# Kernel optimization log

Hardware: AMD Instinct MI355X
Metric: run time of the kernel (lower is better)

## Reference

```python
import jax, jax.numpy as jnp
import numpy as np

N_HEADS = 16
D_MODEL = 2048
D_HEAD = D_MODEL // N_HEADS
B, T = 4, 2048


def setup_inputs() -> dict:
    key = jax.random.key(0)
    k1, k2, k3 = jax.random.split(key, 3)
    x = jax.random.normal(k1, (B, T, D_MODEL), dtype=jnp.float32)
    # stored as [in, out] so y = x @ W + b (equivalent to torch Linear with W_torch = W.T)
    W_qkv = jax.random.normal(k2, (D_MODEL, 3 * D_MODEL), dtype=jnp.float32) * (D_MODEL ** -0.5)
    b_qkv = jnp.zeros((3 * D_MODEL,), dtype=jnp.float32)
    W_out = jax.random.normal(k3, (D_MODEL, D_MODEL), dtype=jnp.float32) * (D_MODEL ** -0.5)
    b_out = jnp.zeros((D_MODEL,), dtype=jnp.float32)
    return {"x": x, "W_qkv": W_qkv, "b_qkv": b_qkv, "W_out": W_out, "b_out": b_out}


def reference(x, W_qkv, b_qkv, W_out, b_out):
    b, t, c = x.shape
    qkv = x @ W_qkv + b_qkv                       # [B,T,3C]
    q, k, v = jnp.split(qkv, 3, axis=-1)
    # [B,T,C] -> [B,H,T,Dh]
    def heads(u):
        return u.reshape(b, t, N_HEADS, D_HEAD).transpose(0, 2, 1, 3)
    q, k, v = heads(q), heads(k), heads(v)
    scale = 1.0 / D_HEAD                          # muP scale: 1/d_head (not 1/sqrt)
    att = jnp.einsum('bhqd,bhkd->bhqk', q, k) * scale
    causal = jnp.tril(jnp.ones((t, t), dtype=bool))
    att = jnp.where(causal, att, -jnp.inf)
    att = jax.nn.softmax(att, axis=-1)
    y = jnp.einsum('bhqk,bhkd->bhqd', att, v)     # [B,H,T,Dh]
    y = y.transpose(0, 2, 1, 3).reshape(b, t, c)
    return y @ W_out + b_out
```

## Files before the change

kernel.cpp:

```cpp
#include <hip/hip_runtime.h>
#include <hip/hip_bf16.h>
#include <cstdint>


using f32x4  = __attribute__((ext_vector_type(4))) float;
using u32x4  = __attribute__((ext_vector_type(4))) unsigned int;
using u16x8  = __attribute__((ext_vector_type(8))) unsigned short;
using u16x4  = __attribute__((ext_vector_type(4))) unsigned short;
using bf16x8 = __attribute__((ext_vector_type(8))) __bf16;

__device__ __forceinline__ unsigned short f2bf(float f) {
  unsigned int u = __builtin_bit_cast(unsigned int, f);
  u += 0x7fffu + ((u >> 16) & 1u);
  return (unsigned short)(u >> 16);
}

__device__ __forceinline__ void async_copy16(const unsigned short* g, unsigned short* l) {
  __builtin_amdgcn_global_load_lds(
      (const __attribute__((address_space(1))) unsigned int*)g,
      (__attribute__((address_space(3))) unsigned int*)l,
      16, 0, 0);
}

__global__ __launch_bounds__(256) void cast_x_kernel(const float* __restrict__ x,
                                                     unsigned short* __restrict__ xb) {
  const size_t i = (size_t)blockIdx.x * 256 + threadIdx.x;
  const float* p = x + i * 8;
  f32x4 a = *(const f32x4*)p;
  f32x4 b = *(const f32x4*)(p + 4);
  u16x8 o;
#pragma unroll
  for (int e = 0; e < 4; ++e) { o[e] = f2bf(a[e]); o[e + 4] = f2bf(b[e]); }
  *(u32x4*)(xb + i * 8) = __builtin_bit_cast(u32x4, o);
}

__global__ __launch_bounds__(256) void transpose_cast_w(const float* __restrict__ W,
                                                        unsigned short* __restrict__ WT,
                                                        int K, int N) {
  __shared__ unsigned short tbuf[64 * 68];
  const int tid = threadIdx.x;
  const int k0 = blockIdx.x * 64, n0 = blockIdx.y * 64;
#pragma unroll
  for (int it = 0; it < 4; ++it) {
    int c = it * 256 + tid;
    int kl = c >> 4, n4 = (c & 15) * 4;
    f32x4 v = *(const f32x4*)(W + (size_t)(k0 + kl) * N + n0 + n4);
#pragma unroll
    for (int e = 0; e < 4; ++e) tbuf[(n4 + e) * 68 + kl] = f2bf(v[e]);
  }
  __syncthreads();
#pragma unroll
  for (int it = 0; it < 2; ++it) {
    int c = it * 256 + tid;
    int nl = c >> 3, k8 = (c & 7) * 8;
    u16x4 lo = *(const u16x4*)&tbuf[nl * 68 + k8];
    u16x4 hi = *(const u16x4*)&tbuf[nl * 68 + k8 + 4];
    u16x8 o;
#pragma unroll
    for (int e = 0; e < 4; ++e) { o[e] = lo[e]; o[e + 4] = hi[e]; }
    *(u32x4*)(WT + (size_t)(n0 + nl) * K + k0 + k8) = __builtin_bit_cast(u32x4, o);
  }
}

__global__ __launch_bounds__(256) void transpose_v_kernel(const unsigned short* __restrict__ qkv,
                                                          unsigned short* __restrict__ vT) {
  __shared__ unsigned short tbuf[64 * 68];
  const int tid = threadIdx.x;
  const int t0 = blockIdx.x * 64;
  const int d0 = blockIdx.y * 64;
  const int bh = blockIdx.z;
  const int b = bh >> 4, h = bh & 15;
#pragma unroll
  for (int it = 0; it < 2; ++it) {
    int c = it * 256 + tid;
    int tl = c >> 3, d8 = (c & 7) * 8;
    u32x4 v = *(const u32x4*)(qkv + (size_t)(b * 2048 + t0 + tl) * 6144 + 4096 + h * 128 + d0 + d8);
    u16x8 u = __builtin_bit_cast(u16x8, v);
#pragma unroll
    for (int e = 0; e < 8; ++e) tbuf[(d8 + e) * 68 + tl] = u[e];
  }
  __syncthreads();
#pragma unroll
  for (int it = 0; it < 2; ++it) {
    int c = it * 256 + tid;
    int dl = c >> 3, t8 = (c & 7) * 8;
    u16x4 lo = *(const u16x4*)&tbuf[dl * 68 + t8];
    u16x4 hi = *(const u16x4*)&tbuf[dl * 68 + t8 + 4];
    u16x8 o;
#pragma unroll
    for (int e = 0; e < 4; ++e) { o[e] = lo[e]; o[e + 4] = hi[e]; }
    *(u32x4*)(vT + ((size_t)bh * 128 + d0 + dl) * 2048 + t0 + t8) = __builtin_bit_cast(u32x4, o);
  }
}


__device__ __forceinline__ void stage_region(const unsigned short* gsrc, int K,
                                             unsigned short* region, int tid) {
#pragma unroll
  for (int l = 0; l < 2; ++l) {
    const int s = l * 512 + tid;
    const int row = s >> 3, c = s & 7;
    const int g = c ^ (row & 7);
    async_copy16(gsrc + (size_t)row * K + g * 8, region + s * 8);
  }
}

__device__ __forceinline__ bf16x8 lds_frag(const unsigned short* region, int row, int ch) {
  return __builtin_bit_cast(bf16x8,
      *(const u32x4*)(region + row * 64 + ((ch ^ (row & 7)) * 8)));
}

template <bool OUT_BF16>
__global__ __launch_bounds__(512, 1) void gemm_bt(const unsigned short* __restrict__ A,
                                                  const unsigned short* __restrict__ BT,
                                                  const float* __restrict__ bias,
                                                  void* __restrict__ Cout,
                                                  int M, int N, int K) {
  __shared__ unsigned short As[32768];
  __shared__ unsigned short Bs[32768];

  const int tid  = threadIdx.x;
  const int lane = tid & 63;
  const int wave = tid >> 6;
  const int r16  = lane & 15;
  const int quad = lane >> 4;
  const int wm   = (wave >> 2) * 128;
  const int wn   = (wave & 3) * 64;
  const int rhA  = wave >> 2;
  const int rhB  = (wave >> 1) & 1;
  const int brow = wn & 64;

  const int orig = blockIdx.y * gridDim.x + blockIdx.x;
  const int xcd  = orig & 7;
  const int kb   = orig >> 3;
  const int MC   = gridDim.x >> 3;
  const int m0   = (xcd * MC + (kb % MC)) * 256;
  const int n0   = (kb / MC) * 256;

  const unsigned short* Ag = A + (size_t)m0 * K;
  const unsigned short* Bg = BT + (size_t)n0 * K;
  const int NT = K >> 6;

  f32x4 acc[8][4] = {};

#pragma unroll
  for (int tt = 0; tt < 2; ++tt) {
    const size_t kk0 = (size_t)tt * 64;
    unsigned short* Ad = As + tt * 16384;
    unsigned short* Bd = Bs + tt * 16384;
    stage_region(Bg + kk0, K, Bd, tid);
    stage_region(Bg + (size_t)128 * K + kk0, K, Bd + 8192, tid);
    stage_region(Ag + kk0, K, Ad, tid);
    stage_region(Ag + (size_t)128 * K + kk0, K, Ad + 8192, tid);
  }
  asm volatile("s_waitcnt vmcnt(8)" ::: "memory");
  __builtin_amdgcn_s_barrier();

  for (int t = 0; t < NT; ++t) {
    const int buf = t & 1;
    const unsigned short* Ar = As + buf * 16384 + rhA * 8192;
    const unsigned short* Br = Bs + buf * 16384 + rhB * 8192;
    unsigned short* Asg = As + buf * 16384;
    unsigned short* Bsg = Bs + buf * 16384;
    const bool pre = (t + 2 < NT);
    const size_t kpre = (size_t)(t + 2) << 6;

    bf16x8 a0[4][2], a1[4][2], b0[2][2], b1[2][2];

#pragma unroll
    for (int mi = 0; mi < 4; ++mi)
#pragma unroll
      for (int kk = 0; kk < 2; ++kk)
        a0[mi][kk] = lds_frag(Ar, mi * 16 + r16, kk * 4 + quad);
#pragma unroll
    for (int nj = 0; nj < 2; ++nj)
#pragma unroll
      for (int kk = 0; kk < 2; ++kk)
        b0[nj][kk] = lds_frag(Br, brow + nj * 16 + r16, kk * 4 + quad);
    __builtin_amdgcn_s_barrier();
    asm volatile("s_waitcnt lgkmcnt(0)" ::: "memory");
    __builtin_amdgcn_sched_barrier(0);
    __builtin_amdgcn_s_setprio(1);
#pragma unroll
    for (int mi = 0; mi < 4; ++mi)
#pragma unroll
      for (int nj = 0; nj < 2; ++nj)
#pragma unroll
        for (int kk = 0; kk < 2; ++kk)
          acc[mi][nj] = __builtin_amdgcn_mfma_f32_16x16x32_bf16(a0[mi][kk], b0[nj][kk], acc[mi][nj], 0, 0, 0);
    __builtin_amdgcn_s_setprio(0);
    __builtin_amdgcn_s_barrier();

#pragma unroll
    for (int nj = 0; nj < 2; ++nj)
#pragma unroll
      for (int kk = 0; kk < 2; ++kk)
        b1[nj][kk] = lds_frag(Br, brow + 32 + nj * 16 + r16, kk * 4 + quad);
    __builtin_amdgcn_s_barrier();
    asm volatile("s_waitcnt lgkmcnt(0)" ::: "memory");
    __builtin_amdgcn_sched_barrier(0);
    __builtin_amdgcn_s_setprio(1);
#pragma unroll
    for (int mi = 0; mi < 4; ++mi)
#pragma unroll
      for (int nj = 0; nj < 2; ++nj)
#pragma unroll
        for (int kk = 0; kk < 2; ++kk)
          acc[mi][nj + 2] = __builtin_amdgcn_mfma_f32_16x16x32_bf16(a0[mi][kk], b1[nj][kk], acc[mi][nj + 2], 0, 0, 0);
    __builtin_amdgcn_s_setprio(0);
    __builtin_amdgcn_s_barrier();

#pragma unroll
    for (int mi = 0; mi < 4; ++mi)
#pragma unroll
      for (int kk = 0; kk < 2; ++kk)
        a1[mi][kk] = lds_frag(Ar, 64 + mi * 16 + r16, kk * 4 + quad);
    if (pre) {
      stage_region(Bg + kpre, K, Bsg, tid);
      stage_region(Bg + (size_t)128 * K + kpre, K, Bsg + 8192, tid);
    }
    __builtin_amdgcn_s_barrier();
    asm volatile("s_waitcnt lgkmcnt(0)" ::: "memory");
    __builtin_amdgcn_sched_barrier(0);
    __builtin_amdgcn_s_setprio(1);
#pragma unroll
    for (int mi = 0; mi < 4; ++mi)
#pragma unroll
      for (int nj = 0; nj < 2; ++nj)
#pragma unroll
        for (int kk = 0; kk < 2; ++kk)
          acc[mi + 4][nj + 2] = __builtin_amdgcn_mfma_f32_16x16x32_bf16(a1[mi][kk], b1[nj][kk], acc[mi + 4][nj + 2], 0, 0, 0);
    __builtin_amdgcn_s_setprio(0);
    __builtin_amdgcn_s_barrier();

    if (pre) {
      stage_region(Ag + kpre, K, Asg, tid);
      stage_region(Ag + (size_t)128 * K + kpre, K, Asg + 8192, tid);
    }
    __builtin_amdgcn_s_barrier();
    __builtin_amdgcn_sched_barrier(0);
    __builtin_amdgcn_s_setprio(1);
#pragma unroll
    for (int mi = 0; mi < 4; ++mi)
#pragma unroll
      for (int nj = 0; nj < 2; ++nj)
#pragma unroll
        for (int kk = 0; kk < 2; ++kk)
          acc[mi + 4][nj] = __builtin_amdgcn_mfma_f32_16x16x32_bf16(a1[mi][kk], b0[nj][kk], acc[mi + 4][nj], 0, 0, 0);
    __builtin_amdgcn_s_setprio(0);
    if (pre) { asm volatile("s_waitcnt vmcnt(8)" ::: "memory"); }
    else     { asm volatile("s_waitcnt vmcnt(0)" ::: "memory"); }
    __builtin_amdgcn_s_barrier();
  }

#pragma unroll
  for (int nj = 0; nj < 4; ++nj) {
    const int n = n0 + wn + nj * 16 + r16;
    const float bv = bias[n];
#pragma unroll
    for (int mi = 0; mi < 8; ++mi) {
      const int mr = m0 + wm + mi * 16 + quad * 4;
#pragma unroll
      for (int r = 0; r < 4; ++r) {
        float v = acc[mi][nj][r] + bv;
        if constexpr (OUT_BF16)
          ((unsigned short*)Cout)[(size_t)(mr + r) * N + n] = f2bf(v);
        else
          ((float*)Cout)[(size_t)(mr + r) * N + n] = v;
      }
    }
  }
}

__global__ __launch_bounds__(256, 2) void attn_kernel(const unsigned short* __restrict__ qkv,
                                                      const unsigned short* __restrict__ vT,
                                                      unsigned short* __restrict__ y) {
  __shared__ unsigned short Ks[64 * 128];
  __shared__ unsigned short Vs[128 * 64];
  __shared__ unsigned short Ps[4][32 * 72];

  const int tid  = threadIdx.x;
  const int lane = tid & 63;
  const int wave = tid >> 6;
  const int r16  = lane & 15;
  const int quad = lane >> 4;
  const int qt   = 15 - blockIdx.y;
  const int q0   = qt * 128;
  const int bh   = blockIdx.x;
  const int b    = bh >> 4, h = bh & 15;
  const int wq0  = q0 + wave * 32;
  unsigned short* pl = Ps[wave];

  bf16x8 aq[2][4];
#pragma unroll
  for (int mi = 0; mi < 2; ++mi) {
    const unsigned short* qp = qkv + (size_t)(b * 2048 + wq0 + mi * 16 + r16) * 6144 + h * 128;
#pragma unroll
    for (int kc = 0; kc < 4; ++kc)
      aq[mi][kc] = __builtin_bit_cast(bf16x8, *(const u32x4*)(qp + kc * 32 + quad * 8));
  }

  f32x4 o[2][8] = {};
  float rs_l[2][4] = {};

  const unsigned short* kbase = qkv + (size_t)b * 2048 * 6144 + 2048 + h * 128;
  const unsigned short* vbase = vT + (size_t)bh * 128 * 2048;
  const int ntiles = 2 * qt + 2;

  const int kg = (tid & 15) ^ (tid >> 4);
  const int vg = (tid & 7) ^ ((tid >> 3) & 7);
  const int krow0 = tid >> 4;
  const int vrow0 = tid >> 3;

  u32x4 kreg[4], vreg[4];

#define ATTN_LOADREGS(KV0)                                                              \
  {                                                                                     \
    _Pragma("unroll")                                                                   \
    for (int it = 0; it < 4; ++it)                                                      \
      kreg[it] = *(const u32x4*)(kbase + (size_t)((KV0) + it * 16 + krow0) * 6144 + kg * 8); \
    _Pragma("unroll")                                                                   \
    for (int it = 0; it < 4; ++it)                                                      \
      vreg[it] = *(const u32x4*)(vbase + (size_t)(it * 32 + vrow0) * 2048 + (KV0) + vg * 8); \
  }

  ATTN_LOADREGS(0);

  for (int t = 0; t < ntiles; ++t) {
    const int kv0 = t * 64;
    asm volatile("s_waitcnt vmcnt(0)" ::: "memory");
    __builtin_amdgcn_s_barrier();
    __builtin_amdgcn_sched_barrier(0);
#pragma unroll
    for (int it = 0; it < 4; ++it)
      *(u32x4*)(Ks + (it * 256 + tid) * 8) = kreg[it];
#pragma unroll
    for (int it = 0; it < 4; ++it)
      *(u32x4*)(Vs + (it * 256 + tid) * 8) = vreg[it];
    asm volatile("s_waitcnt lgkmcnt(0)" ::: "memory");
    if (t + 1 < ntiles) ATTN_LOADREGS(kv0 + 64);
    __builtin_amdgcn_s_barrier();
    __builtin_amdgcn_sched_barrier(0);

    f32x4 s[2][4] = {};
#pragma unroll
    for (int kc = 0; kc < 4; ++kc) {
#pragma unroll
      for (int nt = 0; nt < 4; ++nt) {
        const int krow = nt * 16 + r16;
        const int chunk = kc * 4 + quad;
        bf16x8 bk = __builtin_bit_cast(bf16x8,
            *(const u32x4*)(Ks + (krow * 16 + (chunk ^ (krow & 15))) * 8));
#pragma unroll
        for (int mi = 0; mi < 2; ++mi)
          s[mi][nt] = __builtin_amdgcn_mfma_f32_16x16x32_bf16(aq[mi][kc], bk, s[mi][nt], 0, 0, 0);
      }
    }

    const bool need_mask = (kv0 + 64 > wq0);
#pragma unroll
    for (int mi = 0; mi < 2; ++mi) {
#pragma unroll
      for (int r = 0; r < 4; ++r) {
        const int qg = wq0 + mi * 16 + quad * 4 + r;
        float acc = 0.0f;
#pragma unroll
        for (int nt = 0; nt < 4; ++nt) {
          float e = exp2f(s[mi][nt][r] * 0.0112718764f);
          if (need_mask && (kv0 + nt * 16 + r16 > qg)) e = 0.0f;
          acc += e;
          pl[(mi * 16 + quad * 4 + r) * 72 + nt * 16 + r16] = f2bf(e);
        }
        rs_l[mi][r] += acc;
      }
    }

#pragma unroll
    for (int kc = 0; kc < 2; ++kc) {
      bf16x8 ap[2];
#pragma unroll
      for (int mi = 0; mi < 2; ++mi)
        ap[mi] = __builtin_bit_cast(bf16x8,
            *(const u32x4*)(pl + (mi * 16 + r16) * 72 + kc * 32 + quad * 8));
#pragma unroll
      for (int d = 0; d < 8; ++d) {
        const int drow = d * 16 + r16;
        const int chunk = kc * 4 + quad;
        bf16x8 bv = __builtin_bit_cast(bf16x8,
            *(const u32x4*)(Vs + (drow * 8 + (chunk ^ (drow & 7))) * 8));
#pragma unroll
        for (int mi = 0; mi < 2; ++mi)
          o[mi][d] = __builtin_amdgcn_mfma_f32_16x16x32_bf16(ap[mi], bv, o[mi][d], 0, 0, 0);
      }
    }
  }

#pragma unroll
  for (int mi = 0; mi < 2; ++mi) {
#pragma unroll
    for (int r = 0; r < 4; ++r) {
      float rs = rs_l[mi][r];
#pragma unroll
      for (int off = 8; off >= 1; off >>= 1) rs += __shfl_xor(rs, off);
      const float inv = 1.0f / rs;
      const int qg = wq0 + mi * 16 + quad * 4 + r;
      unsigned short* yp = y + (size_t)(b * 2048 + qg) * 2048 + h * 128;
#pragma unroll
      for (int d = 0; d < 8; ++d)
        yp[d * 16 + r16] = f2bf(o[mi][d][r] * inv);
    }
  }
#undef ATTN_LOADREGS
}

extern "C" void kernel_launch(void* const* d_in, const int* in_sizes, int n_in,
                              void* d_out, int out_size, void* d_ws, size_t ws_size,
                              hipStream_t stream) {
  const float* x     = (const float*)d_in[0];
  const float* W_qkv = (const float*)d_in[1];
  const float* b_qkv = (const float*)d_in[2];
  const float* W_out = (const float*)d_in[3];
  const float* b_out = (const float*)d_in[4];

  unsigned short* ws  = (unsigned short*)d_ws;
  unsigned short* qkv = ws;
  unsigned short* vT  = ws + 50331648;
  unsigned short* xb  = ws + 67108864;
  unsigned short* wqT = ws + 83886080;
  unsigned short* woT = ws + 96468992;
  unsigned short* y   = xb;

  cast_x_kernel<<<8192, 256, 0, stream>>>(x, xb);
  transpose_cast_w<<<dim3(32, 96), 256, 0, stream>>>(W_qkv, wqT, 2048, 6144);
  transpose_cast_w<<<dim3(32, 32), 256, 0, stream>>>(W_out, woT, 2048, 2048);
  gemm_bt<true><<<dim3(32, 24), 512, 0, stream>>>(xb, wqT, b_qkv, qkv, 8192, 6144, 2048);
  transpose_v_kernel<<<dim3(32, 2, 64), 256, 0, stream>>>(qkv, vT);
  attn_kernel<<<dim3(64, 16), 256, 0, stream>>>(qkv, vT, y);
  gemm_bt<false><<<dim3(32, 8), 512, 0, stream>>>(y, woT, b_out, d_out, 8192, 2048, 2048);
}
```

Baseline: 574.4 us.

## Software-pipeline LDS fragment loads across GEMM k-iterations

Restructures the GEMM main loop so the LDS fragment reads for each MFMA phase are issued before the previous phase's MFMAs. Next-iteration a0/b0 fragments are prefetched from the other buffer during the current iteration, and the explicit lgkmcnt waits are dropped. The global-load wait moves earlier (vmcnt(4) after the B prefetch) so the next buffer is ready before its fragments are read. This aims to hide LDS latency behind MFMA work, at the cost of more registers (a0n/b0n) and subtler buffer-hazard ordering.

Measured after the change: 1.222 ms. 2.13x slower.

```diff
diff --git a/kernel.cpp b/kernel.cpp
--- a/kernel.cpp
+++ b/kernel.cpp
@@ -156,30 +156,43 @@
   asm volatile("s_waitcnt vmcnt(8)" ::: "memory");
   __builtin_amdgcn_s_barrier();
 
+  bf16x8 a0[4][2], b0[2][2];
+  {
+    const unsigned short* Ar0 = As + rhA * 8192;
+    const unsigned short* Br0 = Bs + rhB * 8192;
+#pragma unroll
+    for (int mi = 0; mi < 4; ++mi)
+#pragma unroll
+      for (int kk = 0; kk < 2; ++kk)
+        a0[mi][kk] = lds_frag(Ar0, mi * 16 + r16, kk * 4 + quad);
+#pragma unroll
+    for (int nj = 0; nj < 2; ++nj)
+#pragma unroll
+      for (int kk = 0; kk < 2; ++kk)
+        b0[nj][kk] = lds_frag(Br0, brow + nj * 16 + r16, kk * 4 + quad);
+  }
+
   for (int t = 0; t < NT; ++t) {
     const int buf = t & 1;
-    const unsigned short* Ar = As + buf * 16384 + rhA * 8192;
-    const unsigned short* Br = Bs + buf * 16384 + rhB * 8192;
+    const unsigned short* Ar  = As + buf * 16384 + rhA * 8192;
+    const unsigned short* Br  = Bs + buf * 16384 + rhB * 8192;
+    const unsigned short* Arn = As + (buf ^ 1) * 16384 + rhA * 8192;
+    const unsigned short* Brn = Bs + (buf ^ 1) * 16384 + rhB * 8192;
     unsigned short* Asg = As + buf * 16384;
     unsigned short* Bsg = Bs + buf * 16384;
     const bool pre = (t + 2 < NT);
+    const bool nx  = (t + 1 < NT);
     const size_t kpre = (size_t)(t + 2) << 6;
 
-    bf16x8 a0[4][2], a1[4][2], b0[2][2], b1[2][2];
-
-#pragma unroll
-    for (int mi = 0; mi < 4; ++mi)
+    bf16x8 a1[4][2], b1[2][2], a0n[4][2], b0n[2][2];
+
+    __builtin_amdgcn_s_barrier();
+    __builtin_amdgcn_sched_barrier(0);
+#pragma unroll
+    for (int nj = 0; nj < 2; ++nj)
 #pragma unroll
       for (int kk = 0; kk < 2; ++kk)
-        a0[mi][kk] = lds_frag(Ar, mi * 16 + r16, kk * 4 + quad);
-#pragma unroll
-    for (int nj = 0; nj < 2; ++nj)
-#pragma unroll
-      for (int kk = 0; kk < 2; ++kk)
-        b0[nj][kk] = lds_frag(Br, brow + nj * 16 + r16, kk * 4 + quad);
-    __builtin_amdgcn_s_barrier();
-    asm volatile("s_waitcnt lgkmcnt(0)" ::: "memory");
-    __builtin_amdgcn_sched_barrier(0);
+        b1[nj][kk] = lds_frag(Br, brow + 32 + nj * 16 + r16, kk * 4 + quad);
     __builtin_amdgcn_s_setprio(1);
 #pragma unroll
     for (int mi = 0; mi < 4; ++mi)
@@ -189,16 +202,15 @@
         for (int kk = 0; kk < 2; ++kk)
           acc[mi][nj] = __builtin_amdgcn_mfma_f32_16x16x32_bf16(a0[mi][kk], b0[nj][kk], acc[mi][nj], 0, 0, 0);
     __builtin_amdgcn_s_setprio(0);
-    __builtin_amdgcn_s_barrier();
-
-#pragma unroll
-    for (int nj = 0; nj < 2; ++nj)
+    __builtin_amdgcn_sched_barrier(0);
+
+    __builtin_amdgcn_s_barrier();
+    __builtin_amdgcn_sched_barrier(0);
+#pragma unroll
+    for (int mi = 0; mi < 4; ++mi)
 #pragma unroll
       for (int kk = 0; kk < 2; ++kk)
-        b1[nj][kk] = lds_frag(Br, brow + 32 + nj * 16 + r16, kk * 4 + quad);
-    __builtin_amdgcn_s_barrier();
-    asm volatile("s_waitcnt lgkmcnt(0)" ::: "memory");
-    __builtin_amdgcn_sched_barrier(0);
+        a1[mi][kk] = lds_frag(Ar, 64 + mi * 16 + r16, kk * 4 + quad);
     __builtin_amdgcn_s_setprio(1);
 #pragma unroll
     for (int mi = 0; mi < 4; ++mi)
@@ -208,20 +220,26 @@
         for (int kk = 0; kk < 2; ++kk)
           acc[mi][nj + 2] = __builtin_amdgcn_mfma_f32_16x16x32_bf16(a0[mi][kk], b1[nj][kk], acc[mi][nj + 2], 0, 0, 0);
     __builtin_amdgcn_s_setprio(0);
-    __builtin_amdgcn_s_barrier();
-
-#pragma unroll
-    for (int mi = 0; mi < 4; ++mi)
-#pragma unroll
-      for (int kk = 0; kk < 2; ++kk)
-        a1[mi][kk] = lds_frag(Ar, 64 + mi * 16 + r16, kk * 4 + quad);
+    __builtin_amdgcn_sched_barrier(0);
+
+    __builtin_amdgcn_s_barrier();
+    __builtin_amdgcn_sched_barrier(0);
     if (pre) {
       stage_region(Bg + kpre, K, Bsg, tid);
       stage_region(Bg + (size_t)128 * K + kpre, K, Bsg + 8192, tid);
-    }
-    __builtin_amdgcn_s_barrier();
-    asm volatile("s_waitcnt lgkmcnt(0)" ::: "memory");
-    __builtin_amdgcn_sched_barrier(0);
+      asm volatile("s_waitcnt vmcnt(4)" ::: "memory");
+    } else {
+      asm volatile("s_waitcnt vmcnt(0)" ::: "memory");
+    }
+    __builtin_amdgcn_s_barrier();
+    __builtin_amdgcn_sched_barrier(0);
+    if (nx) {
+#pragma unroll
+      for (int nj = 0; nj < 2; ++nj)
+#pragma unroll
+        for (int kk = 0; kk < 2; ++kk)
+          b0n[nj][kk] = lds_frag(Brn, brow + nj * 16 + r16, kk * 4 + quad);
+    }
     __builtin_amdgcn_s_setprio(1);
 #pragma unroll
     for (int mi = 0; mi < 4; ++mi)
@@ -231,14 +249,21 @@
         for (int kk = 0; kk < 2; ++kk)
           acc[mi + 4][nj + 2] = __builtin_amdgcn_mfma_f32_16x16x32_bf16(a1[mi][kk], b1[nj][kk], acc[mi + 4][nj + 2], 0, 0, 0);
     __builtin_amdgcn_s_setprio(0);
-    __builtin_amdgcn_s_barrier();
-
+    __builtin_amdgcn_sched_barrier(0);
+
+    __builtin_amdgcn_s_barrier();
+    __builtin_amdgcn_sched_barrier(0);
     if (pre) {
       stage_region(Ag + kpre, K, Asg, tid);
       stage_region(Ag + (size_t)128 * K + kpre, K, Asg + 8192, tid);
     }
-    __builtin_amdgcn_s_barrier();
-    __builtin_amdgcn_sched_barrier(0);
+    if (nx) {
+#pragma unroll
+      for (int mi = 0; mi < 4; ++mi)
+#pragma unroll
+        for (int kk = 0; kk < 2; ++kk)
+          a0n[mi][kk] = lds_frag(Arn, mi * 16 + r16, kk * 4 + quad);
+    }
     __builtin_amdgcn_s_setprio(1);
 #pragma unroll
     for (int mi = 0; mi < 4; ++mi)
@@ -248,9 +273,20 @@
         for (int kk = 0; kk < 2; ++kk)
           acc[mi + 4][nj] = __builtin_amdgcn_mfma_f32_16x16x32_bf16(a1[mi][kk], b0[nj][kk], acc[mi + 4][nj], 0, 0, 0);
     __builtin_amdgcn_s_setprio(0);
-    if (pre) { asm volatile("s_waitcnt vmcnt(8)" ::: "memory"); }
-    else     { asm volatile("s_waitcnt vmcnt(0)" ::: "memory"); }
-    __builtin_amdgcn_s_barrier();
+    __builtin_amdgcn_sched_barrier(0);
+
+    if (nx) {
+#pragma unroll
+      for (int mi = 0; mi < 4; ++mi)
+#pragma unroll
+        for (int kk = 0; kk < 2; ++kk)
+          a0[mi][kk] = a0n[mi][kk];
+#pragma unroll
+      for (int nj = 0; nj < 2; ++nj)
+#pragma unroll
+        for (int kk = 0; kk < 2; ++kk)
+          b0[nj][kk] = b0n[nj][kk];
+    }
   }
 
 #pragma unroll
```

## Halve GEMM K-tile to 32 and prefetch next-tile fragments across iterations

Applied to the files above, without the earlier changes.

Cuts the GEMM's K step from 64 to 32, which halves LDS buffer size, and changes the swizzle to suit 32-wide rows. The main loop is restructured so the a0/b0 fragments for the next tile are loaded from the other buffer while the current MFMAs run, which removes several barriers and lgkmcnt waits per step. The intent is better overlap of LDS reads and global loads with MFMA work. In exchange the loop runs twice as many iterations with less MFMA work per barrier, and it relies on implicit wait insertion for the LDS reads.

New measurement: 679.7 us. 1.18x slower.

```diff
diff --git a/kernel.cpp b/kernel.cpp
--- a/kernel.cpp
+++ b/kernel.cpp
@@ -94,20 +94,16 @@
 }
 
 
-__device__ __forceinline__ void stage_region(const unsigned short* gsrc, int K,
-                                             unsigned short* region, int tid) {
-#pragma unroll
-  for (int l = 0; l < 2; ++l) {
-    const int s = l * 512 + tid;
-    const int row = s >> 3, c = s & 7;
-    const int g = c ^ (row & 7);
-    async_copy16(gsrc + (size_t)row * K + g * 8, region + s * 8);
-  }
-}
-
-__device__ __forceinline__ bf16x8 lds_frag(const unsigned short* region, int row, int ch) {
-  return __builtin_bit_cast(bf16x8,
-      *(const u32x4*)(region + row * 64 + ((ch ^ (row & 7)) * 8)));
+__device__ __forceinline__ void stage_region32(const unsigned short* gsrc, int K,
+                                               unsigned short* region, int tid) {
+  const int row = tid >> 2, c = tid & 3;
+  const int g = c ^ ((row >> 1) & 3);
+  async_copy16(gsrc + (size_t)row * K + g * 8, region + tid * 8);
+}
+
+__device__ __forceinline__ bf16x8 lds_frag32(const unsigned short* region, int row, int q) {
+  const int ch = q ^ ((row >> 1) & 3);
+  return __builtin_bit_cast(bf16x8, *(const u32x4*)(region + row * 32 + ch * 8));
 }
 
 template <bool OUT_BF16>
@@ -116,8 +112,8 @@
                                                   const float* __restrict__ bias,
                                                   void* __restrict__ Cout,
                                                   int M, int N, int K) {
-  __shared__ unsigned short As[32768];
-  __shared__ unsigned short Bs[32768];
+  __shared__ unsigned short As[16384];
+  __shared__ unsigned short Bs[16384];
 
   const int tid  = threadIdx.x;
   const int lane = tid & 63;
@@ -139,118 +135,114 @@
 
   const unsigned short* Ag = A + (size_t)m0 * K;
   const unsigned short* Bg = BT + (size_t)n0 * K;
-  const int NT = K >> 6;
+  const int NT = K >> 5;
 
   f32x4 acc[8][4] = {};
 
 #pragma unroll
   for (int tt = 0; tt < 2; ++tt) {
-    const size_t kk0 = (size_t)tt * 64;
-    unsigned short* Ad = As + tt * 16384;
-    unsigned short* Bd = Bs + tt * 16384;
-    stage_region(Bg + kk0, K, Bd, tid);
-    stage_region(Bg + (size_t)128 * K + kk0, K, Bd + 8192, tid);
-    stage_region(Ag + kk0, K, Ad, tid);
-    stage_region(Ag + (size_t)128 * K + kk0, K, Ad + 8192, tid);
-  }
-  asm volatile("s_waitcnt vmcnt(8)" ::: "memory");
+    const size_t kk0 = (size_t)tt * 32;
+    unsigned short* Ad = As + tt * 8192;
+    unsigned short* Bd = Bs + tt * 8192;
+    stage_region32(Bg + kk0, K, Bd, tid);
+    stage_region32(Bg + (size_t)128 * K + kk0, K, Bd + 4096, tid);
+    stage_region32(Ag + kk0, K, Ad, tid);
+    stage_region32(Ag + (size_t)128 * K + kk0, K, Ad + 4096, tid);
+  }
+  asm volatile("s_waitcnt vmcnt(4)" ::: "memory");
   __builtin_amdgcn_s_barrier();
+  __builtin_amdgcn_sched_barrier(0);
+
+  bf16x8 a0[4], b0[2];
+#pragma unroll
+  for (int mi = 0; mi < 4; ++mi) a0[mi] = lds_frag32(As + rhA * 4096, mi * 16 + r16, quad);
+#pragma unroll
+  for (int nj = 0; nj < 2; ++nj) b0[nj] = lds_frag32(Bs + rhB * 4096, brow + nj * 16 + r16, quad);
 
   for (int t = 0; t < NT; ++t) {
     const int buf = t & 1;
-    const unsigned short* Ar = As + buf * 16384 + rhA * 8192;
-    const unsigned short* Br = Bs + buf * 16384 + rhB * 8192;
-    unsigned short* Asg = As + buf * 16384;
-    unsigned short* Bsg = Bs + buf * 16384;
+    const unsigned short* Ar  = As + buf * 8192 + rhA * 4096;
+    const unsigned short* Br  = Bs + buf * 8192 + rhB * 4096;
+    const unsigned short* Arn = As + (buf ^ 1) * 8192 + rhA * 4096;
+    const unsigned short* Brn = Bs + (buf ^ 1) * 8192 + rhB * 4096;
+    unsigned short* Asg = As + buf * 8192;
+    unsigned short* Bsg = Bs + buf * 8192;
     const bool pre = (t + 2 < NT);
-    const size_t kpre = (size_t)(t + 2) << 6;
-
-    bf16x8 a0[4][2], a1[4][2], b0[2][2], b1[2][2];
-
+    const bool nx  = (t + 1 < NT);
+    const size_t kpre = (size_t)(t + 2) << 5;
+
+    bf16x8 a1[4], b1[2], a0n[4], b0n[2];
+
+#pragma unroll
+    for (int nj = 0; nj < 2; ++nj) b1[nj] = lds_frag32(Br, brow + 32 + nj * 16 + r16, quad);
+    __builtin_amdgcn_s_setprio(1);
 #pragma unroll
     for (int mi = 0; mi < 4; ++mi)
 #pragma unroll
-      for (int kk = 0; kk < 2; ++kk)
-        a0[mi][kk] = lds_frag(Ar, mi * 16 + r16, kk * 4 + quad);
-#pragma unroll
-    for (int nj = 0; nj < 2; ++nj)
-#pragma unroll
-      for (int kk = 0; kk < 2; ++kk)
-        b0[nj][kk] = lds_frag(Br, brow + nj * 16 + r16, kk * 4 + quad);
+      for (int nj = 0; nj < 2; ++nj)
+        acc[mi][nj] = __builtin_amdgcn_mfma_f32_16x16x32_bf16(a0[mi], b0[nj], acc[mi][nj], 0, 0, 0);
+    __builtin_amdgcn_s_setprio(0);
+
+#pragma unroll
+    for (int mi = 0; mi < 4; ++mi) a1[mi] = lds_frag32(Ar, 64 + mi * 16 + r16, quad);
+    __builtin_amdgcn_s_setprio(1);
+#pragma unroll
+    for (int mi = 0; mi < 4; ++mi)
+#pragma unroll
+      for (int nj = 0; nj < 2; ++nj)
+        acc[mi][nj + 2] = __builtin_amdgcn_mfma_f32_16x16x32_bf16(a0[mi], b1[nj], acc[mi][nj + 2], 0, 0, 0);
+    __builtin_amdgcn_s_setprio(0);
+    __builtin_amdgcn_sched_barrier(0);
+
     __builtin_amdgcn_s_barrier();
-    asm volatile("s_waitcnt lgkmcnt(0)" ::: "memory");
-    __builtin_amdgcn_sched_barrier(0);
+    __builtin_amdgcn_sched_barrier(0);
+    if (pre) {
+      stage_region32(Bg + kpre, K, Bsg, tid);
+      stage_region32(Bg + (size_t)128 * K + kpre, K, Bsg + 4096, tid);
+      asm volatile("s_waitcnt vmcnt(2)" ::: "memory");
+    } else {
+      asm volatile("s_waitcnt vmcnt(0)" ::: "memory");
+    }
+    __builtin_amdgcn_s_barrier();
+    __builtin_amdgcn_sched_barrier(0);
+    if (nx) {
+#pragma unroll
+      for (int nj = 0; nj < 2; ++nj) b0n[nj] = lds_frag32(Brn, brow + nj * 16 + r16, quad);
+    }
     __builtin_amdgcn_s_setprio(1);
 #pragma unroll
     for (int mi = 0; mi < 4; ++mi)
 #pragma unroll
       for (int nj = 0; nj < 2; ++nj)
-#pragma unroll
-        for (int kk = 0; kk < 2; ++kk)
-          acc[mi][nj] = __builtin_amdgcn_mfma_f32_16x16x32_bf16(a0[mi][kk], b0[nj][kk], acc[mi][nj], 0, 0, 0);
+        acc[mi + 4][nj + 2] = __builtin_amdgcn_mfma_f32_16x16x32_bf16(a1[mi], b1[nj], acc[mi + 4][nj + 2], 0, 0, 0);
     __builtin_amdgcn_s_setprio(0);
+    __builtin_amdgcn_sched_barrier(0);
+
     __builtin_amdgcn_s_barrier();
-
-#pragma unroll
-    for (int nj = 0; nj < 2; ++nj)
-#pragma unroll
-      for (int kk = 0; kk < 2; ++kk)
-        b1[nj][kk] = lds_frag(Br, brow + 32 + nj * 16 + r16, kk * 4 + quad);
-    __builtin_amdgcn_s_barrier();
-    asm volatile("s_waitcnt lgkmcnt(0)" ::: "memory");
-    __builtin_amdgcn_sched_barrier(0);
+    __builtin_amdgcn_sched_barrier(0);
+    if (pre) {
+      stage_region32(Ag + kpre, K, Asg, tid);
+      stage_region32(Ag + (size_t)128 * K + kpre, K, Asg + 4096, tid);
+    }
+    if (nx) {
+#pragma unroll
+      for (int mi = 0; mi < 4; ++mi) a0n[mi] = lds_frag32(Arn, mi * 16 + r16, quad);
+    }
     __builtin_amdgcn_s_setprio(1);
 #pragma unroll
     for (int mi = 0; mi < 4; ++mi)
 #pragma unroll
       for (int nj = 0; nj < 2; ++nj)
-#pragma unroll
-        for (int kk = 0; kk < 2; ++kk)
-          acc[mi][nj + 2] = __builtin_amdgcn_mfma_f32_16x16x32_bf16(a0[mi][kk], b1[nj][kk], acc[mi][nj + 2], 0, 0, 0);
+        acc[mi + 4][nj] = __builtin_amdgcn_mfma_f32_16x16x32_bf16(a1[mi], b0[nj], acc[mi + 4][nj], 0, 0, 0);
     __builtin_amdgcn_s_setprio(0);
-    __builtin_amdgcn_s_barrier();
-
-#pragma unroll
-    for (int mi = 0; mi < 4; ++mi)
-#pragma unroll
-      for (int kk = 0; kk < 2; ++kk)
-        a1[mi][kk] = lds_frag(Ar, 64 + mi * 16 + r16, kk * 4 + quad);
-    if (pre) {
-      stage_region(Bg + kpre, K, Bsg, tid);
-      stage_region(Bg + (size_t)128 * K + kpre, K, Bsg + 8192, tid);
-    }
-    __builtin_amdgcn_s_barrier();
-    asm volatile("s_waitcnt lgkmcnt(0)" ::: "memory");
-    __builtin_amdgcn_sched_barrier(0);
-    __builtin_amdgcn_s_setprio(1);
-#pragma unroll
-    for (int mi = 0; mi < 4; ++mi)
-#pragma unroll
-      for (int nj = 0; nj < 2; ++nj)
-#pragma unroll
-        for (int kk = 0; kk < 2; ++kk)
-          acc[mi + 4][nj + 2] = __builtin_amdgcn_mfma_f32_16x16x32_bf16(a1[mi][kk], b1[nj][kk], acc[mi + 4][nj + 2], 0, 0, 0);
-    __builtin_amdgcn_s_setprio(0);
-    __builtin_amdgcn_s_barrier();
-
-    if (pre) {
-      stage_region(Ag + kpre, K, Asg, tid);
-      stage_region(Ag + (size_t)128 * K + kpre, K, Asg + 8192, tid);
-    }
-    __builtin_amdgcn_s_barrier();
-    __builtin_amdgcn_sched_barrier(0);
-    __builtin_amdgcn_s_setprio(1);
-#pragma unroll
-    for (int mi = 0; mi < 4; ++mi)
-#pragma unroll
-      for (int nj = 0; nj < 2; ++nj)
-#pragma unroll
-        for (int kk = 0; kk < 2; ++kk)
-          acc[mi + 4][nj] = __builtin_amdgcn_mfma_f32_16x16x32_bf16(a1[mi][kk], b0[nj][kk], acc[mi + 4][nj], 0, 0, 0);
-    __builtin_amdgcn_s_setprio(0);
-    if (pre) { asm volatile("s_waitcnt vmcnt(8)" ::: "memory"); }
-    else     { asm volatile("s_waitcnt vmcnt(0)" ::: "memory"); }
-    __builtin_amdgcn_s_barrier();
+    __builtin_amdgcn_sched_barrier(0);
+
+    if (nx) {
+#pragma unroll
+      for (int mi = 0; mi < 4; ++mi) a0[mi] = a0n[mi];
+#pragma unroll
+      for (int nj = 0; nj < 2; ++nj) b0[nj] = b0n[nj];
+    }
   }
 
 #pragma unroll
```
